# Optimization experiments

Measured on AMD Instinct MI355X. Metric: run time of the kernel, lower is better.

The kernel has to match this reference:

```python
import jax, jax.numpy as jnp
import numpy as np

N = 50000
E = 800000
NEG_SLOPE = 0.2
BN_EPS = 1e-5


def _gat_conv(x, src, dst, W, a_src, a_dst, bias, heads, out_ch, concat):
    # Linear projection per head: [N, heads, out_ch]
    h = (x @ W).reshape(-1, heads, out_ch)
    # Per-node attention terms alpha_src/alpha_dst: [N, heads]
    al_s = (h * a_src[None]).sum(-1)
    al_d = (h * a_dst[None]).sum(-1)
    # Edge logits with LeakyReLU: [E, heads]
    logits = jax.nn.leaky_relu(al_s[src] + al_d[dst], NEG_SLOPE)
    # Segment (scatter) softmax over edges grouped by destination node
    m = jax.ops.segment_max(logits, dst, num_segments=N)
    e = jnp.exp(logits - m[dst])
    s = jax.ops.segment_sum(e, dst, num_segments=N)
    alpha = e / (s[dst] + 1e-16)                      # [E, heads]
    # Weighted message aggregation: scatter-add to destinations
    msg = h[src] * alpha[:, :, None]                  # [E, heads, out_ch]
    out = jax.ops.segment_sum(msg, dst, num_segments=N)  # [N, heads, out_ch]
    out = out.reshape(-1, heads * out_ch) if concat else out.mean(axis=1)
    return out + bias


def _bn_eval(x, gamma, beta, mean, var):
    return (x - mean) * jax.lax.rsqrt(var + BN_EPS) * gamma + beta


def setup_inputs() -> dict:
    key = jax.random.key(0)
    ks = jax.random.split(key, 12)
    in_ch, hid, heads, out_cls = 128, 64, 2, 40
    return {
        "x": jax.random.normal(ks[0], (N, in_ch), jnp.float32),
        "edge_index": jax.random.randint(ks[1], (2, E), 0, N, jnp.int32),
        "W1": jax.random.normal(ks[2], (in_ch, heads * hid), jnp.float32) * 0.1,
        "a1_src": jax.random.normal(ks[3], (heads, hid), jnp.float32) * 0.1,
        "a1_dst": jax.random.normal(ks[4], (heads, hid), jnp.float32) * 0.1,
        "b1": jnp.zeros((heads * hid,), jnp.float32),
        "bn1_gamma": jnp.ones((heads * hid,), jnp.float32),
        "bn1_beta": jnp.zeros((heads * hid,), jnp.float32),
        "bn1_mean": jax.random.normal(ks[5], (heads * hid,), jnp.float32) * 0.1,
        "bn1_var": jax.random.uniform(ks[6], (heads * hid,), jnp.float32, 0.5, 1.5),
        "W2": jax.random.normal(ks[7], (heads * hid, out_cls), jnp.float32) * 0.1,
        "a2_src": jax.random.normal(ks[8], (1, out_cls), jnp.float32) * 0.1,
        "a2_dst": jax.random.normal(ks[9], (1, out_cls), jnp.float32) * 0.1,
        "b2": jnp.zeros((out_cls,), jnp.float32),
    }


def reference(x, edge_index, W1, a1_src, a1_dst, b1, bn1_gamma, bn1_beta,
              bn1_mean, bn1_var, W2, a2_src, a2_dst, b2):
    # add self loops
    loops = jnp.arange(N, dtype=edge_index.dtype)
    src = jnp.concatenate([edge_index[0], loops])
    dst = jnp.concatenate([edge_index[1], loops])
    # layer 1: GATConv(heads=2, concat) -> BN(eval) -> ReLU (dropout is eval no-op)
    h = _gat_conv(x, src, dst, W1, a1_src, a1_dst, b1, heads=2, out_ch=64, concat=True)
    h = jax.nn.relu(_bn_eval(h, bn1_gamma, bn1_beta, bn1_mean, bn1_var))
    # output layer: GATConv(heads=1, concat=False)
    out = _gat_conv(h, src, dst, W2, a2_src, a2_dst, b2, heads=1, out_ch=40, concat=False)
    return jax.nn.log_softmax(out, axis=1)
```

## Files before the change

kernel.cpp:

```cpp
#include <hip/hip_runtime.h>
#include <hip/hip_bf16.h>

#define NEG_SLOPE 0.2f
#define BN_EPS 1e-5f

#define NBLK 256
#define COARSE_SHIFT 9
#define COARSE_NPB 512

typedef __attribute__((ext_vector_type(8))) short s8v;
typedef __attribute__((ext_vector_type(4))) float f4v;

__device__ __forceinline__ float wred_sum(float v) {
    #pragma unroll
    for (int m = 32; m > 0; m >>= 1) v += __shfl_xor(v, m);
    return v;
}
__device__ __forceinline__ float wred_max(float v) {
    #pragma unroll
    for (int m = 32; m > 0; m >>= 1) v = fmaxf(v, __shfl_xor(v, m));
    return v;
}
__device__ __forceinline__ int wred_isum(int v) {
    #pragma unroll
    for (int m = 32; m > 0; m >>= 1) v += __shfl_xor(v, m);
    return v;
}
__device__ __forceinline__ float xor16_sum(float v) {
    #pragma unroll
    for (int m = 1; m < 16; m <<= 1) v += __shfl_xor(v, m);
    return v;
}

__device__ __forceinline__ unsigned pack_bf16(float a, float b) {
    __hip_bfloat162 t;
    t.x = __float2bfloat16(a);
    t.y = __float2bfloat16(b);
    return *(unsigned*)&t;
}
__device__ __forceinline__ float2 unpack_bf16(unsigned u) {
    __hip_bfloat162 t = *(__hip_bfloat162*)&u;
    return {__bfloat162float(t.x), __bfloat162float(t.y)};
}
__device__ __forceinline__ short bf16s(float f) {
    __hip_bfloat16 h = __float2bfloat16(f);
    return *(short*)&h;
}

__device__ __forceinline__ unsigned enc_ord(float f) {
    unsigned u = __float_as_uint(f);
    return (u & 0x80000000u) ? ~u : (u | 0x80000000u);
}
__device__ __forceinline__ float dec_ord(unsigned e) {
    unsigned u = (e & 0x80000000u) ? (e ^ 0x80000000u) : ~e;
    return __uint_as_float(u);
}

__global__ __launch_bounds__(256) void part_hist(const int* __restrict__ ei, int E, int Et,
                                                 int chunk, int* __restrict__ hist, int nCoarse,
                                                 unsigned* __restrict__ gmax) {
    __shared__ int h[128];
    int b = blockIdx.x, t = threadIdx.x;
    if (b == 0 && t < 4) gmax[t] = 0u;
    if (t < 128) h[t] = 0;
    __syncthreads();
    int beg = b * chunk, end = min(beg + chunk, Et);
    for (int idx = beg + t; idx < end; idx += 256) {
        int d = (idx < E) ? ei[E + idx] : (idx - E);
        atomicAdd(&h[d >> COARSE_SHIFT], 1);
    }
    __syncthreads();
    if (t < nCoarse) hist[t * NBLK + b] = h[t];
}

__global__ __launch_bounds__(1024) void csr_mid(int* __restrict__ hist,
                                                int* __restrict__ cbase, int nCoarse) {
    __shared__ int ctot_s[128];
    __shared__ int scn[128];
    __shared__ int cb_s[129];
    int t = threadIdx.x;
    int wv = t >> 6, ln = t & 63;
    if (t < 128) ctot_s[t] = 0;
    __syncthreads();
    for (int c = wv; c < nCoarse; c += 16) {
        int idx = c * NBLK + 4 * ln;
        int4 v = *(int4*)&hist[idx];
        int s = wred_isum(v.x + v.y + v.z + v.w);
        if (ln == 0) ctot_s[c] = s;
    }
    __syncthreads();
    int v0 = 0;
    if (t < 128) { v0 = ctot_s[t]; scn[t] = v0; }
    __syncthreads();
    for (int off = 1; off < 128; off <<= 1) {
        int u = (t >= off && t < 128) ? scn[t - off] : 0;
        __syncthreads();
        if (t < 128) scn[t] += u;
        __syncthreads();
    }
    if (t < 128) cb_s[t] = scn[t] - v0;
    if (t == 127) cb_s[128] = scn[127];
    __syncthreads();
    if (t <= nCoarse) cbase[t] = cb_s[t];
    for (int c = wv; c < nCoarse; c += 16) {
        int base = cb_s[c];
        int idx = c * NBLK + 4 * ln;
        int4 v = *(int4*)&hist[idx];
        int sl = v.x + v.y + v.z + v.w;
        int inc = sl;
        #pragma unroll
        for (int off = 1; off < 64; off <<= 1) {
            int u = __shfl_up(inc, off);
            if (ln >= off) inc += u;
        }
        int exc = inc - sl + base;
        int4 o;
        o.x = exc;
        o.y = exc + v.x;
        o.z = exc + v.x + v.y;
        o.w = exc + v.x + v.y + v.z;
        *(int4*)&hist[idx] = o;
    }
}

__global__ __launch_bounds__(256) void part_scatter(const int* __restrict__ ei, int E, int Et,
                                                    int chunk, const int* __restrict__ hist,
                                                    unsigned* __restrict__ staged, int nCoarse) {
    __shared__ int cur[128];
    int b = blockIdx.x, t = threadIdx.x;
    if (t < nCoarse) cur[t] = hist[t * NBLK + b];
    __syncthreads();
    int beg = b * chunk, end = min(beg + chunk, Et);
    for (int idx = beg + t; idx < end; idx += 256) {
        int s, d;
        if (idx < E) { s = ei[idx]; d = ei[E + idx]; }
        else         { s = idx - E; d = idx - E; }
        int c = d >> COARSE_SHIFT;
        int pos = atomicAdd(&cur[c], 1);
        staged[pos] = ((unsigned)s << COARSE_SHIFT) | (unsigned)(d & (COARSE_NPB - 1));
    }
}

__global__ __launch_bounds__(512) void fine_place(const unsigned* __restrict__ staged,
                                                  const int* __restrict__ cbase,
                                                  int* __restrict__ offs,
                                                  int* __restrict__ csr, int Nn, int nCoarse) {
    __shared__ int hcnt[COARSE_NPB];
    __shared__ int scn[COARSE_NPB];
    int b = blockIdx.x, t = threadIdx.x;
    int node0 = b << COARSE_SHIFT;
    int nloc = min(COARSE_NPB, Nn - node0);
    hcnt[t] = 0;
    __syncthreads();
    int ebeg = cbase[b], eend = cbase[b + 1];
    for (int p = ebeg + t; p < eend; p += 512) {
        atomicAdd(&hcnt[staged[p] & (COARSE_NPB - 1)], 1);
    }
    __syncthreads();
    int val = hcnt[t];
    scn[t] = val;
    __syncthreads();
    for (int off = 1; off < COARSE_NPB; off <<= 1) {
        int u = (t >= off) ? scn[t - off] : 0;
        __syncthreads();
        scn[t] += u;
        __syncthreads();
    }
    int exc = ebeg + scn[t] - val;
    if (t < nloc) offs[node0 + t] = exc;
    if (b == nCoarse - 1 && t == 0) offs[Nn] = eend;
    hcnt[t] = exc;
    __syncthreads();
    for (int p = ebeg + t; p < eend; p += 512) {
        unsigned v = staged[p];
        int pos = atomicAdd(&hcnt[v & (COARSE_NPB - 1)], 1);
        csr[pos] = (int)(v >> COARSE_SHIFT);
    }
}

__global__ __launch_bounds__(256) void gemm1_mfma(const float* __restrict__ x,
                                                  const float* __restrict__ W,
                                                  const float* __restrict__ a1s,
                                                  const float* __restrict__ a1d,
                                                  unsigned* __restrict__ h1b,
                                                  float* __restrict__ als,
                                                  float* __restrict__ ald, int Nn) {
    __shared__ __align__(16) char smem[33792];
    short* fragtab = (short*)smem;
    float* lout    = (float*)smem;

    int t = threadIdx.x;
    int br = blockIdx.x * 64;

    #pragma unroll
    for (int i = 0; i < 8; ++i) {
        int s   = t + 256 * i;
        int grp = s >> 6;
        int ls  = s & 63;
        int ct = grp >> 2, kc = grp & 3;
        int nn = ls & 15, quad = ls >> 4;
        int kb = kc * 32 + quad * 8;
        int cc = ct * 16 + nn;
        #pragma unroll
        for (int j = 0; j < 8; ++j)
            fragtab[s * 8 + j] = bf16s(W[(size_t)(kb + j) * 128 + cc]);
    }
    __syncthreads();

    int w    = t >> 6;
    int lane = t & 63;
    int nn   = lane & 15;
    int quad = lane >> 4;
    int rowbase = br + w * 16;
    int arow = min(rowbase + nn, Nn - 1);
    const float* xr = x + (size_t)arow * 128;

    f4v acc[8];
    #pragma unroll
    for (int ct = 0; ct < 8; ++ct) acc[ct] = (f4v){0.f, 0.f, 0.f, 0.f};

    #pragma unroll
    for (int kc = 0; kc < 4; ++kc) {
        float4 v0 = *(const float4*)(xr + kc * 32 + quad * 8);
        float4 v1 = *(const float4*)(xr + kc * 32 + quad * 8 + 4);
        union { s8v s; uint4 u; } A;
        A.u.x = pack_bf16(v0.x, v0.y); A.u.y = pack_bf16(v0.z, v0.w);
        A.u.z = pack_bf16(v1.x, v1.y); A.u.w = pack_bf16(v1.z, v1.w);
        #pragma unroll
        for (int ct = 0; ct < 8; ++ct) {
            s8v B = *(s8v*)(fragtab + (size_t)((ct * 4 + kc) * 64 + lane) * 8);
            acc[ct] = __builtin_amdgcn_mfma_f32_16x16x32_bf16(A.s, B, acc[ct], 0, 0, 0);
        }
    }

    float s_c[8], d_c[8];
    #pragma unroll
    for (int ct = 0; ct < 8; ++ct) {
        s_c[ct] = a1s[ct * 16 + nn];
        d_c[ct] = a1d[ct * 16 + nn];
    }
    #pragma unroll
    for (int reg = 0; reg < 4; ++reg) {
        float ps0 = 0.f, pd0 = 0.f, ps1 = 0.f, pd1 = 0.f;
        #pragma unroll
        for (int ct = 0; ct < 4; ++ct) { ps0 += acc[ct][reg] * s_c[ct]; pd0 += acc[ct][reg] * d_c[ct]; }
        #pragma unroll
        for (int ct = 4; ct < 8; ++ct) { ps1 += acc[ct][reg] * s_c[ct]; pd1 += acc[ct][reg] * d_c[ct]; }
        ps0 = xor16_sum(ps0); pd0 = xor16_sum(pd0);
        ps1 = xor16_sum(ps1); pd1 = xor16_sum(pd1);
        int r = rowbase + quad * 4 + reg;
        if (nn == 0 && r < Nn) {
            als[(size_t)r * 2]     = ps0;
            als[(size_t)r * 2 + 1] = ps1;
            ald[(size_t)r * 2]     = pd0;
            ald[(size_t)r * 2 + 1] = pd1;
        }
    }

    __syncthreads();
    #pragma unroll
    for (int ct = 0; ct < 8; ++ct)
        #pragma unroll
        for (int reg = 0; reg < 4; ++reg)
            lout[w * 2112 + (quad * 4 + reg) * 132 + ct * 16 + nn] = acc[ct][reg];
    int row_l = lane >> 2;
    int ch    = lane & 3;
    int r = rowbase + row_l;
    if (r < Nn) {
        const float* src = lout + w * 2112 + row_l * 132 + ch * 32;
        #pragma unroll
        for (int i = 0; i < 4; ++i) {
            uint4 pk = {pack_bf16(src[8 * i + 0], src[8 * i + 1]),
                        pack_bf16(src[8 * i + 2], src[8 * i + 3]),
                        pack_bf16(src[8 * i + 4], src[8 * i + 5]),
                        pack_bf16(src[8 * i + 6], src[8 * i + 7])};
            *(uint4*)(h1b + (size_t)r * 64 + ch * 16 + i * 4) = pk;
        }
    }
}

template <int H>
__global__ __launch_bounds__(256) void almax_kernel(const float* __restrict__ als,
                                                    unsigned* __restrict__ gmax, int off, int Nn,
                                                    const float* __restrict__ b1,
                                                    const float* __restrict__ g1,
                                                    const float* __restrict__ be1,
                                                    const float* __restrict__ mn1,
                                                    const float* __restrict__ vr1,
                                                    float* __restrict__ bnscale,
                                                    float* __restrict__ bnshift) {
    __shared__ float red[4][H];
    int t = threadIdx.x;
    if (bnscale && blockIdx.x == 0 && t < 128) {
        float sc = rsqrtf(vr1[t] + BN_EPS) * g1[t];
        bnscale[t] = sc;
        bnshift[t] = be1[t] + (b1[t] - mn1[t]) * sc;
    }
    float m[H];
    #pragma unroll
    for (int h = 0; h < H; ++h) m[h] = -1e30f;
    for (int n = blockIdx.x * 256 + t; n < Nn; n += gridDim.x * 256) {
        #pragma unroll
        for (int h = 0; h < H; ++h) m[h] = fmaxf(m[h], als[n * H + h]);
    }
    #pragma unroll
    for (int h = 0; h < H; ++h) m[h] = wred_max(m[h]);
    int wid = t >> 6;
    if ((t & 63) == 0) {
        #pragma unroll
        for (int h = 0; h < H; ++h) red[wid][h] = m[h];
    }
    __syncthreads();
    if (t == 0) {
        #pragma unroll
        for (int h = 0; h < H; ++h) {
            float mm = fmaxf(fmaxf(red[0][h], red[1][h]), fmaxf(red[2][h], red[3][h]));
            atomicMax(&gmax[off + h], enc_ord(mm));
        }
    }
}

__global__ __launch_bounds__(256) void softagg1_kernel(const int* __restrict__ offs, const int* __restrict__ csr,
                            const unsigned* __restrict__ h1b,
                            const float* __restrict__ als, const float* __restrict__ ald,
                            const unsigned* __restrict__ gmax,
                            const float* __restrict__ bnscale, const float* __restrict__ bnshift,
                            unsigned* __restrict__ hbnb, int Nn) {
    __shared__ int   sh_s[4][4][16];
    __shared__ float sh_e[4][4][2][16];
    int wid = threadIdx.x >> 6, lane = threadIdx.x & 63;
    int g = lane >> 4;
    int l = lane & 15;
    int head = l >> 3;
    int n = blockIdx.x * 16 + wid * 4 + g;
    if (n >= Nn) return;
    int b = offs[n], e = offs[n + 1];
    float2 aldn = *(const float2*)(ald + (size_t)n * 2);
    float bd0 = dec_ord(gmax[0]) + aldn.x; bd0 = (bd0 > 0.f) ? bd0 : NEG_SLOPE * bd0;
    float bd1 = dec_ord(gmax[1]) + aldn.y; bd1 = (bd1 > 0.f) ? bd1 : NEG_SLOPE * bd1;

    float acc[8];
    #pragma unroll
    for (int j = 0; j < 8; ++j) acc[j] = 0.f;
    float den0 = 0.f, den1 = 0.f;

    for (int base = b; base < e; base += 16) {
        int cnt = min(16, e - base);
        int   s1 = 0;
        float e0r = 0.f, e1r = 0.f;
        if (l < cnt) {
            s1 = csr[base + l];
            float2 as = *(const float2*)(als + (size_t)s1 * 2);
            float l0 = as.x + aldn.x; l0 = (l0 > 0.f) ? l0 : NEG_SLOPE * l0;
            float l1 = as.y + aldn.y; l1 = (l1 > 0.f) ? l1 : NEG_SLOPE * l1;
            e0r = __expf(l0 - bd0);
            e1r = __expf(l1 - bd1);
            den0 += e0r; den1 += e1r;
        }
        sh_s[wid][g][l]    = s1;
        sh_e[wid][g][0][l] = e0r;
        sh_e[wid][g][1][l] = e1r;
        int i = 0;
        for (; i + 1 < cnt; i += 2) {
            int   sA  = sh_s[wid][g][i];
            int   sB  = sh_s[wid][g][i + 1];
            float evA = sh_e[wid][g][head][i];
            float evB = sh_e[wid][g][head][i + 1];
            uint4 vA = *(const uint4*)(h1b + (size_t)sA * 64 + 4 * l);
            uint4 vB = *(const uint4*)(h1b + (size_t)sB * 64 + 4 * l);
            float2 f;
            f = unpack_bf16(vA.x); acc[0] += f.x * evA; acc[1] += f.y * evA;
            f = unpack_bf16(vA.y); acc[2] += f.x * evA; acc[3] += f.y * evA;
            f = unpack_bf16(vA.z); acc[4] += f.x * evA; acc[5] += f.y * evA;
            f = unpack_bf16(vA.w); acc[6] += f.x * evA; acc[7] += f.y * evA;
            f = unpack_bf16(vB.x); acc[0] += f.x * evB; acc[1] += f.y * evB;
            f = unpack_bf16(vB.y); acc[2] += f.x * evB; acc[3] += f.y * evB;
            f = unpack_bf16(vB.z); acc[4] += f.x * evB; acc[5] += f.y * evB;
            f = unpack_bf16(vB.w); acc[6] += f.x * evB; acc[7] += f.y * evB;
        }
        if (i < cnt) {
            int   s  = sh_s[wid][g][i];
            float ev = sh_e[wid][g][head][i];
            uint4 v = *(const uint4*)(h1b + (size_t)s * 64 + 4 * l);
            float2 f;
            f = unpack_bf16(v.x); acc[0] += f.x * ev; acc[1] += f.y * ev;
            f = unpack_bf16(v.y); acc[2] += f.x * ev; acc[3] += f.y * ev;
            f = unpack_bf16(v.z); acc[4] += f.x * ev; acc[5] += f.y * ev;
            f = unpack_bf16(v.w); acc[6] += f.x * ev; acc[7] += f.y * ev;
        }
    }
    #pragma unroll
    for (int m = 1; m < 16; m <<= 1) {
        den0 += __shfl_xor(den0, m);
        den1 += __shfl_xor(den1, m);
    }
    float inv = 1.f / ((head ? den1 : den0) + 1e-16f);
    int c = 8 * l;
    float4 sa = *(const float4*)(bnscale + c), sb = *(const float4*)(bnscale + c + 4);
    float4 ha = *(const float4*)(bnshift + c), hb = *(const float4*)(bnshift + c + 4);
    float o0 = fmaxf(acc[0] * inv * sa.x + ha.x, 0.f);
    float o1 = fmaxf(acc[1] * inv * sa.y + ha.y, 0.f);
    float o2 = fmaxf(acc[2] * inv * sa.z + ha.z, 0.f);
    float o3 = fmaxf(acc[3] * inv * sa.w + ha.w, 0.f);
    float o4 = fmaxf(acc[4] * inv * sb.x + hb.x, 0.f);
    float o5 = fmaxf(acc[5] * inv * sb.y + hb.y, 0.f);
    float o6 = fmaxf(acc[6] * inv * sb.z + hb.z, 0.f);
    float o7 = fmaxf(acc[7] * inv * sb.w + hb.w, 0.f);
    uint4 pk = {pack_bf16(o0, o1), pack_bf16(o2, o3), pack_bf16(o4, o5), pack_bf16(o6, o7)};
    *(uint4*)(hbnb + (size_t)n * 64 + 4 * l) = pk;
}

__global__ __launch_bounds__(256) void gemm2_tiled(const unsigned* __restrict__ hbnb,
                                                   const float* __restrict__ W2,
                                                   const float* __restrict__ a2s,
                                                   const float* __restrict__ a2d,
                                                   unsigned* __restrict__ h2b,
                                                   float* __restrict__ als, float* __restrict__ ald,
                                                   int Nn) {
    __shared__ float Ast[32][132];
    __shared__ float Bs[32][68];
    int t  = threadIdx.x;
    int tx = t & 15;
    int ty = t >> 4;
    int br = blockIdx.x * 128;

    float as4[4], ad4[4];
    #pragma unroll
    for (int j = 0; j < 4; ++j) {
        int c = 4 * tx + j;
        as4[j] = (c < 40) ? a2s[c] : 0.f;
        ad4[j] = (c < 40) ? a2d[c] : 0.f;
    }

    float acc[8][4];
    #pragma unroll
    for (int i = 0; i < 8; ++i)
        #pragma unroll
        for (int j = 0; j < 4; ++j) acc[i][j] = 0.f;

    int k4   = t & 7;
    int rowA = t >> 3;

    for (int k0 = 0; k0 < 128; k0 += 32) {
        #pragma unroll
        for (int i = 0; i < 4; ++i) {
            int r  = rowA + 32 * i;
            int gr = min(br + r, Nn - 1);
            uint2 v2 = *(const uint2*)(hbnb + (size_t)gr * 64 + (k0 >> 1) + 2 * k4);
            float2 f0 = unpack_bf16(v2.x), f1 = unpack_bf16(v2.y);
            Ast[4 * k4 + 0][r] = f0.x; Ast[4 * k4 + 1][r] = f0.y;
            Ast[4 * k4 + 2][r] = f1.x; Ast[4 * k4 + 3][r] = f1.y;
        }
        #pragma unroll
        for (int i = 0; i < 2; ++i) {
            int f  = t + 256 * i;
            int kk = f >> 4, c4 = f & 15;
            float4 v = {0.f, 0.f, 0.f, 0.f};
            if (c4 < 10) v = *(const float4*)(W2 + (size_t)(k0 + kk) * 40 + 4 * c4);
            *(float4*)&Bs[kk][4 * c4] = v;
        }
        __syncthreads();
        #pragma unroll 8
        for (int kk = 0; kk < 32; ++kk) {
            float4 a0 = *(const float4*)&Ast[kk][8 * ty];
            float4 a1 = *(const float4*)&Ast[kk][8 * ty + 4];
            float4 b0 = *(const float4*)&Bs[kk][4 * tx];
            float av[8] = {a0.x, a0.y, a0.z, a0.w, a1.x, a1.y, a1.z, a1.w};
            #pragma unroll
            for (int i = 0; i < 8; ++i) {
                acc[i][0] += av[i] * b0.x; acc[i][1] += av[i] * b0.y;
                acc[i][2] += av[i] * b0.z; acc[i][3] += av[i] * b0.w;
            }
        }
        __syncthreads();
    }

    #pragma unroll
    for (int i = 0; i < 8; ++i) {
        int r = br + 8 * ty + i;
        if (r < Nn && tx < 10) {
            uint2 pk = {pack_bf16(acc[i][0], acc[i][1]), pack_bf16(acc[i][2], acc[i][3])};
            *(uint2*)(h2b + (size_t)r * 20 + 2 * tx) = pk;
        }
        float ps = acc[i][0] * as4[0] + acc[i][1] * as4[1] + acc[i][2] * as4[2] + acc[i][3] * as4[3];
        float pd = acc[i][0] * ad4[0] + acc[i][1] * ad4[1] + acc[i][2] * ad4[2] + acc[i][3] * ad4[3];
        float sS = xor16_sum(ps);
        float sD = xor16_sum(pd);
        if (tx == 0 && r < Nn) { als[r] = sS; ald[r] = sD; }
    }
}

__global__ __launch_bounds__(256) void softagg2_kernel(const int* __restrict__ offs, const int* __restrict__ csr,
                            const unsigned* __restrict__ h2b,
                            const float* __restrict__ als, const float* __restrict__ ald,
                            const unsigned* __restrict__ gmax,
                            const float* __restrict__ b2,
                            float* __restrict__ out, int Nn) {
    __shared__ int   sh_s[4][8][8];
    __shared__ float sh_ev[4][8][8];
    int wid = threadIdx.x >> 6, lane = threadIdx.x & 63;
    int g = lane >> 3;
    int l = lane & 7;
    int n = blockIdx.x * 32 + wid * 8 + g;
    if (n >= Nn) return;
    int b = offs[n], e = offs[n + 1];
    float aldn = ald[n];
    float bound = dec_ord(gmax[2]) + aldn;
    bound = (bound > 0.f) ? bound : NEG_SLOPE * bound;

    float acc[8];
    #pragma unroll
    for (int j = 0; j < 8; ++j) acc[j] = 0.f;
    float den = 0.f;

    for (int base = b; base < e; base += 8) {
        int cnt = min(8, e - base);
        int   s1 = 0;
        float evr = 0.f;
        if (l < cnt) {
            s1 = csr[base + l];
            float lv = als[s1] + aldn;
            lv = (lv > 0.f) ? lv : NEG_SLOPE * lv;
            evr = __expf(lv - bound);
            den += evr;
        }
        sh_s[wid][g][l]  = s1;
        sh_ev[wid][g][l] = evr;
        if (l < 5) {
            int i = 0;
            for (; i + 1 < cnt; i += 2) {
                int   sA  = sh_s[wid][g][i];
                int   sB  = sh_s[wid][g][i + 1];
                float evA = sh_ev[wid][g][i];
                float evB = sh_ev[wid][g][i + 1];
                uint4 vA = *(const uint4*)(h2b + (size_t)sA * 20 + 4 * l);
                uint4 vB = *(const uint4*)(h2b + (size_t)sB * 20 + 4 * l);
                float2 f;
                f = unpack_bf16(vA.x); acc[0] += f.x * evA; acc[1] += f.y * evA;
                f = unpack_bf16(vA.y); acc[2] += f.x * evA; acc[3] += f.y * evA;
                f = unpack_bf16(vA.z); acc[4] += f.x * evA; acc[5] += f.y * evA;
                f = unpack_bf16(vA.w); acc[6] += f.x * evA; acc[7] += f.y * evA;
                f = unpack_bf16(vB.x); acc[0] += f.x * evB; acc[1] += f.y * evB;
                f = unpack_bf16(vB.y); acc[2] += f.x * evB; acc[3] += f.y * evB;
                f = unpack_bf16(vB.z); acc[4] += f.x * evB; acc[5] += f.y * evB;
                f = unpack_bf16(vB.w); acc[6] += f.x * evB; acc[7] += f.y * evB;
            }
            if (i < cnt) {
                int   s  = sh_s[wid][g][i];
                float ev = sh_ev[wid][g][i];
                uint4 v = *(const uint4*)(h2b + (size_t)s * 20 + 4 * l);
                float2 f;
                f = unpack_bf16(v.x); acc[0] += f.x * ev; acc[1] += f.y * ev;
                f = unpack_bf16(v.y); acc[2] += f.x * ev; acc[3] += f.y * ev;
                f = unpack_bf16(v.z); acc[4] += f.x * ev; acc[5] += f.y * ev;
                f = unpack_bf16(v.w); acc[6] += f.x * ev; acc[7] += f.y * ev;
            }
        }
    }
    #pragma unroll
    for (int m = 1; m < 8; m <<= 1) den += __shfl_xor(den, m);
    float inv = 1.f / (den + 1e-16f);
    bool valid = (l < 5);
    float vv[8];
    float lmax = -1e30f;
    if (valid) {
        int c = 8 * l;
        #pragma unroll
        for (int j = 0; j < 8; ++j) {
            vv[j] = acc[j] * inv + b2[c + j];
            lmax = fmaxf(lmax, vv[j]);
        }
    }
    float m = lmax;
    #pragma unroll
    for (int mm = 1; mm < 8; mm <<= 1) m = fmaxf(m, __shfl_xor(m, mm));
    float es = 0.f;
    if (valid) {
        #pragma unroll
        for (int j = 0; j < 8; ++j) es += __expf(vv[j] - m);
    }
    #pragma unroll
    for (int mm = 1; mm < 8; mm <<= 1) es += __shfl_xor(es, mm);
    float lse = m + logf(es);
    if (valid) {
        float4 oa = {vv[0] - lse, vv[1] - lse, vv[2] - lse, vv[3] - lse};
        float4 ob = {vv[4] - lse, vv[5] - lse, vv[6] - lse, vv[7] - lse};
        *(float4*)(out + (size_t)n * 40 + 8 * l)     = oa;
        *(float4*)(out + (size_t)n * 40 + 8 * l + 4) = ob;
    }
}

extern "C" void kernel_launch(void* const* d_in, const int* in_sizes, int n_in,
                              void* d_out, int out_size, void* d_ws, size_t ws_size,
                              hipStream_t stream) {
    const float* x    = (const float*)d_in[0];
    const int*   ei   = (const int*)d_in[1];
    const float* W1   = (const float*)d_in[2];
    const float* a1s  = (const float*)d_in[3];
    const float* a1d  = (const float*)d_in[4];
    const float* b1   = (const float*)d_in[5];
    const float* g1   = (const float*)d_in[6];
    const float* be1  = (const float*)d_in[7];
    const float* mn1  = (const float*)d_in[8];
    const float* vr1  = (const float*)d_in[9];
    const float* W2   = (const float*)d_in[10];
    const float* a2s  = (const float*)d_in[11];
    const float* a2d  = (const float*)d_in[12];
    const float* b2   = (const float*)d_in[13];
    float* out = (float*)d_out;

    const int N  = in_sizes[0] / 128;
    const int E  = in_sizes[1] / 2;
    const int Et = E + N;
    const int nCoarse = (N + COARSE_NPB - 1) >> COARSE_SHIFT;
    const int chunk   = (Et + NBLK - 1) / NBLK;

    char* p = (char*)d_ws;
    auto alloc = [&](size_t bytes) -> void* {
        void* r = (void*)p;
        p += (bytes + 255) & ~(size_t)255;
        return r;
    };
    int*      hist   = (int*)alloc((size_t)nCoarse * NBLK * 4);
    int*      cbase  = (int*)alloc((size_t)(nCoarse + 1) * 4);
    int*      offs   = (int*)alloc((size_t)(N + 1) * 4);
    unsigned* staged = (unsigned*)alloc((size_t)Et * 4);
    int*      csr    = (int*)alloc((size_t)Et * 4);
    unsigned* h1b    = (unsigned*)alloc((size_t)N * 64 * 4);
    float*    al1sv  = (float*)alloc((size_t)N * 2 * 4);
    float*    al1dv  = (float*)alloc((size_t)N * 2 * 4);
    unsigned* hbnb   = (unsigned*)alloc((size_t)N * 64 * 4);
    unsigned* h2b    = (unsigned*)alloc((size_t)N * 20 * 4);
    float*    al2sv  = (float*)alloc((size_t)N * 4);
    float*    al2dv  = (float*)alloc((size_t)N * 4);
    unsigned* gmax   = (unsigned*)alloc(4 * 4);
    float*    bnscale= (float*)alloc(128 * 4);
    float*    bnshift= (float*)alloc(128 * 4);
    (void)ws_size;

    part_hist<<<NBLK, 256, 0, stream>>>(ei, E, Et, chunk, hist, nCoarse, gmax);
    csr_mid<<<1, 1024, 0, stream>>>(hist, cbase, nCoarse);
    part_scatter<<<NBLK, 256, 0, stream>>>(ei, E, Et, chunk, hist, staged, nCoarse);
    fine_place<<<nCoarse, 512, 0, stream>>>(staged, cbase, offs, csr, N, nCoarse);

    gemm1_mfma<<<(N + 63) / 64, 256, 0, stream>>>(x, W1, a1s, a1d, h1b, al1sv, al1dv, N);
    almax_kernel<2><<<64, 256, 0, stream>>>(al1sv, gmax, 0, N, b1, g1, be1, mn1, vr1, bnscale, bnshift);
    softagg1_kernel<<<(N + 15) / 16, 256, 0, stream>>>(offs, csr, h1b, al1sv, al1dv, gmax,
                                                       bnscale, bnshift, hbnb, N);

    gemm2_tiled<<<(N + 127) / 128, 256, 0, stream>>>(hbnb, W2, a2s, a2d, h2b, al2sv, al2dv, N);
    almax_kernel<1><<<64, 256, 0, stream>>>(al2sv, gmax, 2, N, nullptr, nullptr, nullptr, nullptr,
                                            nullptr, nullptr, nullptr);
    softagg2_kernel<<<(N + 31) / 32, 256, 0, stream>>>(offs, csr, h2b, al2sv, al2dv, gmax, b2, out, N);
}
```

Baseline: 225.2 us.

## Merge gemm1 with partition histogram and CSR scan with attention max

The layer-1 projection GEMM and the destination histogram now share one launch: extra blocks past the GEMM grid build the coarse histogram. The single-block CSR prefix scan is likewise merged with the layer-1 alpha max reduction and the BN constant setup into one 65-block launch. This removes two kernel launches and lets independent work overlap across CUs. In exchange the merged scan block runs with 256 threads instead of 1024, and the layer-2 max kernel is specialised to a single head.

```diff
diff --git a/kernel.cpp b/kernel.cpp
--- a/kernel.cpp
+++ b/kernel.cpp
@@ -56,70 +56,210 @@
     return __uint_as_float(u);
 }
 
-__global__ __launch_bounds__(256) void part_hist(const int* __restrict__ ei, int E, int Et,
-                                                 int chunk, int* __restrict__ hist, int nCoarse,
-                                                 unsigned* __restrict__ gmax) {
-    __shared__ int h[128];
-    int b = blockIdx.x, t = threadIdx.x;
-    if (b == 0 && t < 4) gmax[t] = 0u;
-    if (t < 128) h[t] = 0;
-    __syncthreads();
-    int beg = b * chunk, end = min(beg + chunk, Et);
-    for (int idx = beg + t; idx < end; idx += 256) {
-        int d = (idx < E) ? ei[E + idx] : (idx - E);
-        atomicAdd(&h[d >> COARSE_SHIFT], 1);
-    }
-    __syncthreads();
-    if (t < nCoarse) hist[t * NBLK + b] = h[t];
-}
-
-__global__ __launch_bounds__(1024) void csr_mid(int* __restrict__ hist,
-                                                int* __restrict__ cbase, int nCoarse) {
-    __shared__ int ctot_s[128];
-    __shared__ int scn[128];
-    __shared__ int cb_s[129];
+__global__ __launch_bounds__(256) void k1_gemm1_hist(const float* __restrict__ x,
+                                                     const float* __restrict__ W,
+                                                     const float* __restrict__ a1s,
+                                                     const float* __restrict__ a1d,
+                                                     unsigned* __restrict__ h1b,
+                                                     float* __restrict__ als,
+                                                     float* __restrict__ ald, int Nn, int nGemmB,
+                                                     const int* __restrict__ ei, int E, int Et,
+                                                     int chunk, int* __restrict__ hist, int nCoarse,
+                                                     unsigned* __restrict__ gmax) {
+    __shared__ __align__(16) char smem[33792];
     int t = threadIdx.x;
-    int wv = t >> 6, ln = t & 63;
-    if (t < 128) ctot_s[t] = 0;
-    __syncthreads();
-    for (int c = wv; c < nCoarse; c += 16) {
-        int idx = c * NBLK + 4 * ln;
-        int4 v = *(int4*)&hist[idx];
-        int s = wred_isum(v.x + v.y + v.z + v.w);
-        if (ln == 0) ctot_s[c] = s;
-    }
-    __syncthreads();
-    int v0 = 0;
-    if (t < 128) { v0 = ctot_s[t]; scn[t] = v0; }
-    __syncthreads();
-    for (int off = 1; off < 128; off <<= 1) {
-        int u = (t >= off && t < 128) ? scn[t - off] : 0;
-        __syncthreads();
-        if (t < 128) scn[t] += u;
-        __syncthreads();
-    }
-    if (t < 128) cb_s[t] = scn[t] - v0;
-    if (t == 127) cb_s[128] = scn[127];
-    __syncthreads();
-    if (t <= nCoarse) cbase[t] = cb_s[t];
-    for (int c = wv; c < nCoarse; c += 16) {
-        int base = cb_s[c];
-        int idx = c * NBLK + 4 * ln;
-        int4 v = *(int4*)&hist[idx];
-        int sl = v.x + v.y + v.z + v.w;
-        int inc = sl;
-        #pragma unroll
-        for (int off = 1; off < 64; off <<= 1) {
-            int u = __shfl_up(inc, off);
-            if (ln >= off) inc += u;
-        }
-        int exc = inc - sl + base;
-        int4 o;
-        o.x = exc;
-        o.y = exc + v.x;
-        o.z = exc + v.x + v.y;
-        o.w = exc + v.x + v.y + v.z;
-        *(int4*)&hist[idx] = o;
+
+    if (blockIdx.x >= nGemmB) {
+        int* h = (int*)smem;
+        int b = blockIdx.x - nGemmB;
+        if (b == 0 && t < 4) gmax[t] = 0u;
+        if (t < 128) h[t] = 0;
+        __syncthreads();
+        int beg = b * chunk, end = min(beg + chunk, Et);
+        for (int idx = beg + t; idx < end; idx += 256) {
+            int d = (idx < E) ? ei[E + idx] : (idx - E);
+            atomicAdd(&h[d >> COARSE_SHIFT], 1);
+        }
+        __syncthreads();
+        if (t < nCoarse) hist[t * NBLK + b] = h[t];
+        return;
+    }
+
+    short* fragtab = (short*)smem;
+    float* lout    = (float*)smem;
+    int br = blockIdx.x * 64;
+
+    #pragma unroll
+    for (int i = 0; i < 8; ++i) {
+        int s   = t + 256 * i;
+        int grp = s >> 6;
+        int ls  = s & 63;
+        int ct = grp >> 2, kc = grp & 3;
+        int nn = ls & 15, quad = ls >> 4;
+        int kb = kc * 32 + quad * 8;
+        int cc = ct * 16 + nn;
+        #pragma unroll
+        for (int j = 0; j < 8; ++j)
+            fragtab[s * 8 + j] = bf16s(W[(size_t)(kb + j) * 128 + cc]);
+    }
+    __syncthreads();
+
+    int w    = t >> 6;
+    int lane = t & 63;
+    int nn   = lane & 15;
+    int quad = lane >> 4;
+    int rowbase = br + w * 16;
+    int arow = min(rowbase + nn, Nn - 1);
+    const float* xr = x + (size_t)arow * 128;
+
+    f4v acc[8];
+    #pragma unroll
+    for (int ct = 0; ct < 8; ++ct) acc[ct] = (f4v){0.f, 0.f, 0.f, 0.f};
+
+    #pragma unroll
+    for (int kc = 0; kc < 4; ++kc) {
+        float4 v0 = *(const float4*)(xr + kc * 32 + quad * 8);
+        float4 v1 = *(const float4*)(xr + kc * 32 + quad * 8 + 4);
+        union { s8v s; uint4 u; } A;
+        A.u.x = pack_bf16(v0.x, v0.y); A.u.y = pack_bf16(v0.z, v0.w);
+        A.u.z = pack_bf16(v1.x, v1.y); A.u.w = pack_bf16(v1.z, v1.w);
+        #pragma unroll
+        for (int ct = 0; ct < 8; ++ct) {
+            s8v B = *(s8v*)(fragtab + (size_t)((ct * 4 + kc) * 64 + lane) * 8);
+            acc[ct] = __builtin_amdgcn_mfma_f32_16x16x32_bf16(A.s, B, acc[ct], 0, 0, 0);
+        }
+    }
+
+    float s_c[8], d_c[8];
+    #pragma unroll
+    for (int ct = 0; ct < 8; ++ct) {
+        s_c[ct] = a1s[ct * 16 + nn];
+        d_c[ct] = a1d[ct * 16 + nn];
+    }
+    #pragma unroll
+    for (int reg = 0; reg < 4; ++reg) {
+        float ps0 = 0.f, pd0 = 0.f, ps1 = 0.f, pd1 = 0.f;
+        #pragma unroll
+        for (int ct = 0; ct < 4; ++ct) { ps0 += acc[ct][reg] * s_c[ct]; pd0 += acc[ct][reg] * d_c[ct]; }
+        #pragma unroll
+        for (int ct = 4; ct < 8; ++ct) { ps1 += acc[ct][reg] * s_c[ct]; pd1 += acc[ct][reg] * d_c[ct]; }
+        ps0 = xor16_sum(ps0); pd0 = xor16_sum(pd0);
+        ps1 = xor16_sum(ps1); pd1 = xor16_sum(pd1);
+        int r = rowbase + quad * 4 + reg;
+        if (nn == 0 && r < Nn) {
+            als[(size_t)r * 2]     = ps0;
+            als[(size_t)r * 2 + 1] = ps1;
+            ald[(size_t)r * 2]     = pd0;
+            ald[(size_t)r * 2 + 1] = pd1;
+        }
+    }
+
+    __syncthreads();
+    #pragma unroll
+    for (int ct = 0; ct < 8; ++ct)
+        #pragma unroll
+        for (int reg = 0; reg < 4; ++reg)
+            lout[w * 2112 + (quad * 4 + reg) * 132 + ct * 16 + nn] = acc[ct][reg];
+    int row_l = lane >> 2;
+    int ch    = lane & 3;
+    int r = rowbase + row_l;
+    if (r < Nn) {
+        const float* src = lout + w * 2112 + row_l * 132 + ch * 32;
+        #pragma unroll
+        for (int i = 0; i < 4; ++i) {
+            uint4 pk = {pack_bf16(src[8 * i + 0], src[8 * i + 1]),
+                        pack_bf16(src[8 * i + 2], src[8 * i + 3]),
+                        pack_bf16(src[8 * i + 4], src[8 * i + 5]),
+                        pack_bf16(src[8 * i + 6], src[8 * i + 7])};
+            *(uint4*)(h1b + (size_t)r * 64 + ch * 16 + i * 4) = pk;
+        }
+    }
+}
+
+__global__ __launch_bounds__(256) void k2_mid_almax(int* __restrict__ hist,
+                                                    int* __restrict__ cbase, int nCoarse,
+                                                    const float* __restrict__ als,
+                                                    unsigned* __restrict__ gmax, int Nn,
+                                                    const float* __restrict__ b1,
+                                                    const float* __restrict__ g1,
+                                                    const float* __restrict__ be1,
+                                                    const float* __restrict__ mn1,
+                                                    const float* __restrict__ vr1,
+                                                    float* __restrict__ bnscale,
+                                                    float* __restrict__ bnshift) {
+    __shared__ int s_ct[128];
+    __shared__ int s_sc[128];
+    __shared__ int s_cb[129];
+    __shared__ float red[4][2];
+    int t = threadIdx.x;
+
+    if (blockIdx.x == 0) {
+        int wv = t >> 6, ln = t & 63;
+        if (t < 128) s_ct[t] = 0;
+        __syncthreads();
+        for (int c = wv; c < nCoarse; c += 4) {
+            int idx = c * NBLK + 4 * ln;
+            int4 v = *(int4*)&hist[idx];
+            int s = wred_isum(v.x + v.y + v.z + v.w);
+            if (ln == 0) s_ct[c] = s;
+        }
+        __syncthreads();
+        int v0 = 0;
+        if (t < 128) { v0 = s_ct[t]; s_sc[t] = v0; }
+        __syncthreads();
+        for (int off = 1; off < 128; off <<= 1) {
+            int u = (t >= off && t < 128) ? s_sc[t - off] : 0;
+            __syncthreads();
+            if (t < 128) s_sc[t] += u;
+            __syncthreads();
+        }
+        if (t < 128) s_cb[t] = s_sc[t] - v0;
+        if (t == 127) s_cb[128] = s_sc[127];
+        __syncthreads();
+        if (t <= nCoarse) cbase[t] = s_cb[t];
+        for (int c = wv; c < nCoarse; c += 4) {
+            int base = s_cb[c];
+            int idx = c * NBLK + 4 * ln;
+            int4 v = *(int4*)&hist[idx];
+            int sl = v.x + v.y + v.z + v.w;
+            int inc = sl;
+            #pragma unroll
+            for (int off = 1; off < 64; off <<= 1) {
+                int u = __shfl_up(inc, off);
+                if (ln >= off) inc += u;
+            }
+            int exc = inc - sl + base;
+            int4 o;
+            o.x = exc;
+            o.y = exc + v.x;
+            o.z = exc + v.x + v.y;
+            o.w = exc + v.x + v.y + v.z;
+            *(int4*)&hist[idx] = o;
+        }
+        return;
+    }
+
+    int vb = blockIdx.x - 1;
+    if (bnscale && vb == 0 && t < 128) {
+        float sc = rsqrtf(vr1[t] + BN_EPS) * g1[t];
+        bnscale[t] = sc;
+        bnshift[t] = be1[t] + (b1[t] - mn1[t]) * sc;
+    }
+    float m0 = -1e30f, m1 = -1e30f;
+    for (int n = vb * 256 + t; n < Nn; n += 64 * 256) {
+        m0 = fmaxf(m0, als[n * 2]);
+        m1 = fmaxf(m1, als[n * 2 + 1]);
+    }
+    m0 = wred_max(m0);
+    m1 = wred_max(m1);
+    int wid = t >> 6;
+    if ((t & 63) == 0) { red[wid][0] = m0; red[wid][1] = m1; }
+    __syncthreads();
+    if (t == 0) {
+        float a = fmaxf(fmaxf(red[0][0], red[1][0]), fmaxf(red[2][0], red[3][0]));
+        float b = fmaxf(fmaxf(red[0][1], red[1][1]), fmaxf(red[2][1], red[3][1]));
+        atomicMax(&gmax[0], enc_ord(a));
+        atomicMax(&gmax[1], enc_ord(b));
     }
 }
 
@@ -178,145 +318,20 @@
     }
 }
 
-__global__ __launch_bounds__(256) void gemm1_mfma(const float* __restrict__ x,
-                                                  const float* __restrict__ W,
-                                                  const float* __restrict__ a1s,
-                                                  const float* __restrict__ a1d,
-                                                  unsigned* __restrict__ h1b,
-                                                  float* __restrict__ als,
-                                                  float* __restrict__ ald, int Nn) {
-    __shared__ __align__(16) char smem[33792];
-    short* fragtab = (short*)smem;
-    float* lout    = (float*)smem;
-
+__global__ __launch_bounds__(256) void almax1_kernel(const float* __restrict__ als,
+                                                     unsigned* __restrict__ gmax, int Nn) {
+    __shared__ float red[4];
     int t = threadIdx.x;
-    int br = blockIdx.x * 64;
-
-    #pragma unroll
-    for (int i = 0; i < 8; ++i) {
-        int s   = t + 256 * i;
-        int grp = s >> 6;
-        int ls  = s & 63;
-        int ct = grp >> 2, kc = grp & 3;
-        int nn = ls & 15, quad = ls >> 4;
-        int kb = kc * 32 + quad * 8;
-        int cc = ct * 16 + nn;
-        #pragma unroll
-        for (int j = 0; j < 8; ++j)
-            fragtab[s * 8 + j] = bf16s(W[(size_t)(kb + j) * 128 + cc]);
-    }
-    __syncthreads();
-
-    int w    = t >> 6;
-    int lane = t & 63;
-    int nn   = lane & 15;
-    int quad = lane >> 4;
-    int rowbase = br + w * 16;
-    int arow = min(rowbase + nn, Nn - 1);
-    const float* xr = x + (size_t)arow * 128;
-
-    f4v acc[8];
-    #pragma unroll
-    for (int ct = 0; ct < 8; ++ct) acc[ct] = (f4v){0.f, 0.f, 0.f, 0.f};
-
-    #pragma unroll
-    for (int kc = 0; kc < 4; ++kc) {
-        float4 v0 = *(const float4*)(xr + kc * 32 + quad * 8);
-        float4 v1 = *(const float4*)(xr + kc * 32 + quad * 8 + 4);
-        union { s8v s; uint4 u; } A;
-        A.u.x = pack_bf16(v0.x, v0.y); A.u.y = pack_bf16(v0.z, v0.w);
-        A.u.z = pack_bf16(v1.x, v1.y); A.u.w = pack_bf16(v1.z, v1.w);
-        #pragma unroll
-        for (int ct = 0; ct < 8; ++ct) {
-            s8v B = *(s8v*)(fragtab + (size_t)((ct * 4 + kc) * 64 + lane) * 8);
-            acc[ct] = __builtin_amdgcn_mfma_f32_16x16x32_bf16(A.s, B, acc[ct], 0, 0, 0);
-        }
-    }
-
-    float s_c[8], d_c[8];
-    #pragma unroll
-    for (int ct = 0; ct < 8; ++ct) {
-        s_c[ct] = a1s[ct * 16 + nn];
-        d_c[ct] = a1d[ct * 16 + nn];
-    }
-    #pragma unroll
-    for (int reg = 0; reg < 4; ++reg) {
-        float ps0 = 0.f, pd0 = 0.f, ps1 = 0.f, pd1 = 0.f;
-        #pragma unroll
-        for (int ct = 0; ct < 4; ++ct) { ps0 += acc[ct][reg] * s_c[ct]; pd0 += acc[ct][reg] * d_c[ct]; }
-        #pragma unroll
-        for (int ct = 4; ct < 8; ++ct) { ps1 += acc[ct][reg] * s_c[ct]; pd1 += acc[ct][reg] * d_c[ct]; }
-        ps0 = xor16_sum(ps0); pd0 = xor16_sum(pd0);
-        ps1 = xor16_sum(ps1); pd1 = xor16_sum(pd1);
-        int r = rowbase + quad * 4 + reg;
-        if (nn == 0 && r < Nn) {
-            als[(size_t)r * 2]     = ps0;
-            als[(size_t)r * 2 + 1] = ps1;
-            ald[(size_t)r * 2]     = pd0;
-            ald[(size_t)r * 2 + 1] = pd1;
-        }
-    }
-
-    __syncthreads();
-    #pragma unroll
-    for (int ct = 0; ct < 8; ++ct)
-        #pragma unroll
-        for (int reg = 0; reg < 4; ++reg)
-            lout[w * 2112 + (quad * 4 + reg) * 132 + ct * 16 + nn] = acc[ct][reg];
-    int row_l = lane >> 2;
-    int ch    = lane & 3;
-    int r = rowbase + row_l;
-    if (r < Nn) {
-        const float* src = lout + w * 2112 + row_l * 132 + ch * 32;
-        #pragma unroll
-        for (int i = 0; i < 4; ++i) {
-            uint4 pk = {pack_bf16(src[8 * i + 0], src[8 * i + 1]),
-                        pack_bf16(src[8 * i + 2], src[8 * i + 3]),
-                        pack_bf16(src[8 * i + 4], src[8 * i + 5]),
-                        pack_bf16(src[8 * i + 6], src[8 * i + 7])};
-            *(uint4*)(h1b + (size_t)r * 64 + ch * 16 + i * 4) = pk;
-        }
-    }
-}
-
-template <int H>
-__global__ __launch_bounds__(256) void almax_kernel(const float* __restrict__ als,
-                                                    unsigned* __restrict__ gmax, int off, int Nn,
-                                                    const float* __restrict__ b1,
-                                                    const float* __restrict__ g1,
-                                                    const float* __restrict__ be1,
-                                                    const float* __restrict__ mn1,
-                                                    const float* __restrict__ vr1,
-                                                    float* __restrict__ bnscale,
-                                                    float* __restrict__ bnshift) {
-    __shared__ float red[4][H];
-    int t = threadIdx.x;
-    if (bnscale && blockIdx.x == 0 && t < 128) {
-        float sc = rsqrtf(vr1[t] + BN_EPS) * g1[t];
-        bnscale[t] = sc;
-        bnshift[t] = be1[t] + (b1[t] - mn1[t]) * sc;
-    }
-    float m[H];
-    #pragma unroll
-    for (int h = 0; h < H; ++h) m[h] = -1e30f;
-    for (int n = blockIdx.x * 256 + t; n < Nn; n += gridDim.x * 256) {
-        #pragma unroll
-        for (int h = 0; h < H; ++h) m[h] = fmaxf(m[h], als[n * H + h]);
-    }
-    #pragma unroll
-    for (int h = 0; h < H; ++h) m[h] = wred_max(m[h]);
+    float m = -1e30f;
+    for (int n = blockIdx.x * 256 + t; n < Nn; n += gridDim.x * 256)
+        m = fmaxf(m, als[n]);
+    m = wred_max(m);
     int wid = t >> 6;
-    if ((t & 63) == 0) {
-        #pragma unroll
-        for (int h = 0; h < H; ++h) red[wid][h] = m[h];
-    }
+    if ((t & 63) == 0) red[wid] = m;
     __syncthreads();
     if (t == 0) {
-        #pragma unroll
-        for (int h = 0; h < H; ++h) {
-            float mm = fmaxf(fmaxf(red[0][h], red[1][h]), fmaxf(red[2][h], red[3][h]));
-            atomicMax(&gmax[off + h], enc_ord(mm));
-        }
+        float mm = fmaxf(fmaxf(red[0], red[1]), fmaxf(red[2], red[3]));
+        atomicMax(&gmax[2], enc_ord(mm));
     }
 }
 
@@ -614,6 +629,7 @@
     const int Et = E + N;
     const int nCoarse = (N + COARSE_NPB - 1) >> COARSE_SHIFT;
     const int chunk   = (Et + NBLK - 1) / NBLK;
+    const int nGemmB  = (N + 63) / 64;
 
     char* p = (char*)d_ws;
     auto alloc = [&](size_t bytes) -> void* {
@@ -638,18 +654,17 @@
     float*    bnshift= (float*)alloc(128 * 4);
     (void)ws_size;
 
-    part_hist<<<NBLK, 256, 0, stream>>>(ei, E, Et, chunk, hist, nCoarse, gmax);
-    csr_mid<<<1, 1024, 0, stream>>>(hist, cbase, nCoarse);
+    k1_gemm1_hist<<<nGemmB + NBLK, 256, 0, stream>>>(x, W1, a1s, a1d, h1b, al1sv, al1dv, N, nGemmB,
+                                                     ei, E, Et, chunk, hist, nCoarse, gmax);
+    k2_mid_almax<<<65, 256, 0, stream>>>(hist, cbase, nCoarse, al1sv, gmax, N,
+                                         b1, g1, be1, mn1, vr1, bnscale, bnshift);
     part_scatter<<<NBLK, 256, 0, stream>>>(ei, E, Et, chunk, hist, staged, nCoarse);
     fine_place<<<nCoarse, 512, 0, stream>>>(staged, cbase, offs, csr, N, nCoarse);
 
-    gemm1_mfma<<<(N + 63) / 64, 256, 0, stream>>>(x, W1, a1s, a1d, h1b, al1sv, al1dv, N);
-    almax_kernel<2><<<64, 256, 0, stream>>>(al1sv, gmax, 0, N, b1, g1, be1, mn1, vr1, bnscale, bnshift);
     softagg1_kernel<<<(N + 15) / 16, 256, 0, stream>>>(offs, csr, h1b, al1sv, al1dv, gmax,
                                                        bnscale, bnshift, hbnb, N);
 
     gemm2_tiled<<<(N + 127) / 128, 256, 0, stream>>>(hbnb, W2, a2s, a2d, h2b, al2sv, al2dv, N);
-    almax_kernel<1><<<64, 256, 0, stream>>>(al2sv, gmax, 2, N, nullptr, nullptr, nullptr, nullptr,
-                                            nullptr, nullptr, nullptr);
+    almax1_kernel<<<64, 256, 0, stream>>>(al2sv, gmax, N);
     softagg2_kernel<<<(N + 31) / 32, 256, 0, stream>>>(offs, csr, h2b, al2sv, al2dv, gmax, b2, out, N);
 }
```

Result: no change. 226.9 us (+0.7%).
